# Kernel optimization log

Measured on AMD Instinct MI355X. Metric: run time of the kernel, lower is better.

Reference implementation:

```python
import jax, jax.numpy as jnp
import numpy as np

N = 4096      # number of nodes
C = 8         # channels (w1..w8 in source)
IN_DIM = 256  # input feature dim
D = 64        # per-channel dim (c_dim)
OUT = 128     # out_dim
ITERS = 4     # routing iterations
BETA = 1.0    # temperature
DENSITY = 0.01


def _l2norm(x):
    # tf.nn.l2_normalize along last axis with eps=1e-12
    return x * jax.lax.rsqrt(jnp.maximum(jnp.sum(x * x, axis=-1, keepdims=True), 1e-12))


def setup_inputs() -> dict:
    key = jax.random.key(0)
    k0, k1, k2, k3, k4, k5 = jax.random.split(key, 6)
    features = jax.random.normal(k0, (N, IN_DIM), dtype=jnp.float32)
    # sparse-ish 0/1 adjacency stored densely (as in the original model)
    adj = (jax.random.uniform(k1, (N, N)) < DENSITY).astype(jnp.float32)
    W = jax.random.normal(k2, (C, IN_DIM, D), dtype=jnp.float32)    # w1..w8 stacked
    b = jax.random.normal(k3, (C, 1, D), dtype=jnp.float32)         # b1..b8 stacked
    W_o = jax.random.normal(k4, (C * D, OUT), dtype=jnp.float32)
    bias = jax.random.normal(k5, (1, OUT), dtype=jnp.float32)
    return {"features": features, "adj": adj, "W": W, "b": b, "W_o": W_o, "bias": bias}


def reference(features, adj, W, b, W_o, bias):
    mask = adj > 0  # [N, N]
    # per-channel projection + l2 normalize: z[c] = l2norm(features @ w[c] + b[c])
    z = _l2norm(jnp.einsum('ni,cid->cnd', features, W) + b)  # [C, N, D]
    for _ in range(ITERS):
        # dense per-channel attention (XX^T), masked by adjacency
        A = jnp.einsum('cnd,cmd->cnm', z, z)                 # [C, N, N]
        A = jnp.where(mask[None], A, 0.0) / BETA
        # softmax across channels at each (i, j), then re-mask
        A = jax.nn.softmax(A, axis=0)
        A = jnp.where(mask[None], A, 0.0)
        # aggregate + residual + l2 normalize
        z = _l2norm(z + jnp.einsum('cnm,cmd->cnd', A, z))
    # concat channels along feature axis: [N, C*D]
    h = jnp.transpose(z, (1, 0, 2)).reshape(N, C * D)
    # (dropout skipped: stochastic op, identity in the deterministic reference)
    return h @ W_o + bias
```

## Files before the change

kernel.cpp:

```cpp
#include <hip/hip_runtime.h>
#include <hip/hip_bf16.h>

#define N_NODES 4096
#define C_CH    8
#define IN_DIM  256
#define D_DIM   64
#define CD      512
#define OUT_DIM 128
#define ITERS   4
#define STRIDE  128

typedef __hip_bfloat16 bf16;
typedef short short8 __attribute__((ext_vector_type(8)));
typedef float floatx4 __attribute__((ext_vector_type(4)));

__device__ __forceinline__ float bf2f(bf16 x) { return __bfloat162float(x); }

__device__ __forceinline__ unsigned f2b_rne(float x) {
    unsigned u = __float_as_uint(x);
    return (u + 0x7FFFu + ((u >> 16) & 1u)) >> 16;
}
__device__ __forceinline__ unsigned pack2bf(float a, float b) {
    return f2b_rne(a) | (f2b_rne(b) << 16);
}
__device__ __forceinline__ void unpack2(unsigned v, float& a, float& b) {
    a = __uint_as_float(v << 16);
    b = __uint_as_float(v & 0xFFFF0000u);
}
__device__ __forceinline__ short8 as_s8(uint4 u) {
    union { uint4 a; short8 b; } x; x.a = u; return x.b;
}

__device__ __forceinline__ bool wave_detect(const unsigned* __restrict__ feat_u) {
    int lane = threadIdx.x & 63;
    unsigned u = feat_u[lane];
    int e = (u >> 7) & 0xFF;
    int vote = (e >= 0x68 && e <= 0x86) ? 1 : 0;
    #pragma unroll
    for (int off = 32; off; off >>= 1) vote += __shfl_xor(vote, off);
    return vote >= 32;
}

__global__ __launch_bounds__(256) void mega_pre(
        const void* __restrict__ feat, const void* __restrict__ adj,
        const void* __restrict__ W, const void* __restrict__ b,
        const void* __restrict__ Wo,
        unsigned* __restrict__ zbf, int* __restrict__ deg,
        int* __restrict__ col_buf, unsigned short* __restrict__ Wo_t) {
    bool isbf = wave_detect((const unsigned*)feat);
    int bx = blockIdx.x;
    int t = threadIdx.x;

    if (bx < 512) {
        int nb = bx * 8;
        __shared__ float fs[8 * IN_DIM];
        if (isbf) {
            const uint4* p = (const uint4*)((const unsigned short*)feat + (size_t)nb * IN_DIM);
            uint4 u = p[t];
            float v[8];
            unpack2(u.x, v[0], v[1]); unpack2(u.y, v[2], v[3]);
            unpack2(u.z, v[4], v[5]); unpack2(u.w, v[6], v[7]);
            *(float4*)&fs[t * 8]     = make_float4(v[0], v[1], v[2], v[3]);
            *(float4*)&fs[t * 8 + 4] = make_float4(v[4], v[5], v[6], v[7]);
        } else {
            const float4* p = (const float4*)((const float*)feat + (size_t)nb * IN_DIM);
            float4 u0 = p[t];
            float4 u1 = p[t + 256];
            *(float4*)&fs[t * 4]         = u0;
            *(float4*)&fs[(t + 256) * 4] = u1;
        }
        __syncthreads();

        int d = t & 63;
        size_t wbase0 = (size_t)(t >> 6) * IN_DIM * D_DIM + d;
        size_t wbase1 = (size_t)(4 + (t >> 6)) * IN_DIM * D_DIM + d;
        float a0[8] = {}, a1[8] = {};
        for (int k = 0; k < IN_DIM; k++) {
            float w0, w1;
            if (isbf) {
                w0 = bf2f(((const bf16*)W)[wbase0 + k * D_DIM]);
                w1 = bf2f(((const bf16*)W)[wbase1 + k * D_DIM]);
            } else {
                w0 = ((const float*)W)[wbase0 + k * D_DIM];
                w1 = ((const float*)W)[wbase1 + k * D_DIM];
            }
            #pragma unroll
            for (int r = 0; r < 8; r++) {
                float f = fs[r * IN_DIM + k];
                a0[r] = fmaf(f, w0, a0[r]);
                a1[r] = fmaf(f, w1, a1[r]);
            }
        }
        float b0 = isbf ? bf2f(((const bf16*)b)[t])       : ((const float*)b)[t];
        float b1 = isbf ? bf2f(((const bf16*)b)[256 + t]) : ((const float*)b)[256 + t];

        #pragma unroll
        for (int r = 0; r < 8; r++) {
            float v0 = a0[r] + b0;
            float v1 = a1[r] + b1;
            float ss0 = v0 * v0, ss1 = v1 * v1;
            #pragma unroll
            for (int off = 32; off; off >>= 1) {
                ss0 += __shfl_xor(ss0, off);
                ss1 += __shfl_xor(ss1, off);
            }
            float o0 = v0 * __builtin_amdgcn_rsqf(fmaxf(ss0, 1e-12f));
            float o1 = v1 * __builtin_amdgcn_rsqf(fmaxf(ss1, 1e-12f));
            size_t row = (size_t)(nb + r);
            float p0 = __shfl_xor(o0, 1);
            float p1 = __shfl_xor(o1, 1);
            if (!(t & 1)) {
                zbf[row * 256 + (t >> 1)]       = pack2bf(o0, p0);
                zbf[row * 256 + 128 + (t >> 1)] = pack2bf(o1, p1);
            }
        }
    } else if (bx < 1536) {
        int w = t >> 6, lane = t & 63;
        int i = (bx - 512) * 4 + w;
        int base_out = i * STRIDE;
        int running = 0;
        int nch = isbf ? 8 : 16;
        for (int ch = 0; ch < nch; ch++) {
            unsigned bits = 0;
            int j0, nelem;
            if (isbf) {
                const uint4* p = (const uint4*)((const unsigned short*)adj + (size_t)i * N_NODES);
                uint4 u = p[ch * 64 + lane];
                j0 = (ch * 64 + lane) * 8; nelem = 8;
                unsigned short h[8] = {
                    (unsigned short)(u.x & 0xFFFF), (unsigned short)(u.x >> 16),
                    (unsigned short)(u.y & 0xFFFF), (unsigned short)(u.y >> 16),
                    (unsigned short)(u.z & 0xFFFF), (unsigned short)(u.z >> 16),
                    (unsigned short)(u.w & 0xFFFF), (unsigned short)(u.w >> 16)};
                #pragma unroll
                for (int k = 0; k < 8; k++)
                    if ((h[k] & 0x8000) == 0 && h[k] != 0) bits |= (1u << k);
            } else {
                const float4* p = (const float4*)((const float*)adj + (size_t)i * N_NODES);
                float4 f = p[ch * 64 + lane];
                j0 = (ch * 64 + lane) * 4; nelem = 4;
                if (f.x > 0.f) bits |= 1u;
                if (f.y > 0.f) bits |= 2u;
                if (f.z > 0.f) bits |= 4u;
                if (f.w > 0.f) bits |= 8u;
            }
            int cnt = __popc(bits);
            int sc = cnt;
            #pragma unroll
            for (int off = 1; off < 64; off <<= 1) {
                int v = __shfl_up(sc, off);
                if (lane >= off) sc += v;
            }
            int tot = __shfl(sc, 63);
            int pos = base_out + running + (sc - cnt);
            for (int k = 0; k < nelem; k++) {
                if ((bits >> k) & 1u) {
                    if (pos < base_out + STRIDE) col_buf[pos] = j0 + k;
                    pos++;
                }
            }
            running += tot;
        }
        if ((t & 63) == 0) deg[i] = (running < STRIDE) ? running : STRIDE;
    } else {
        int idx = (bx - 1536) * 256 + t;
        int n = idx & 127;
        int k = idx >> 7;
        unsigned short v;
        if (isbf) v = ((const unsigned short*)Wo)[idx];
        else      v = (unsigned short)f2b_rne(((const float*)Wo)[idx]);
        Wo_t[n * CD + k] = v;
    }
}

__device__ __forceinline__ void edge_step(const float zi[8], float acc[8], uint4 u) {
    float vj[8];
    unpack2(u.x, vj[0], vj[1]);
    unpack2(u.y, vj[2], vj[3]);
    unpack2(u.z, vj[4], vj[5]);
    unpack2(u.w, vj[6], vj[7]);
    float p = 0.f;
    #pragma unroll
    for (int k = 0; k < 8; k++) p = fmaf(zi[k], vj[k], p);
    p += __shfl_xor(p, 1); p += __shfl_xor(p, 2); p += __shfl_xor(p, 4);
    float ex = __expf(p);
    float s = ex;
    s += __shfl_xor(s, 8); s += __shfl_xor(s, 16); s += __shfl_xor(s, 32);
    float wgt = ex * __builtin_amdgcn_rcpf(s);
    #pragma unroll
    for (int k = 0; k < 8; k++) acc[k] = fmaf(wgt, vj[k], acc[k]);
}

__global__ __launch_bounds__(256) void route_kernel(
        const unsigned* __restrict__ zbf_in, unsigned* __restrict__ zbf_out,
        const int* __restrict__ deg, const int* __restrict__ col_buf) {
    int w = threadIdx.x >> 6, lane = threadIdx.x & 63;
    int pair = w >> 1;
    int half = w & 1;
    int i = blockIdx.x * 2 + pair;
    int g = lane >> 3, s = lane & 7;
    __shared__ int   s_cols[2][STRIDE];
    __shared__ float s_acc[2][CD];

    s_cols[pair][half * 64 + lane] = col_buf[i * STRIDE + half * 64 + lane];
    __syncthreads();

    int frag = g * 32 + s * 4;
    uint4 uown = *(const uint4*)(zbf_in + (size_t)i * 256 + frag);
    float zi[8], acc[8];
    unpack2(uown.x, zi[0], zi[1]); unpack2(uown.y, zi[2], zi[3]);
    unpack2(uown.z, zi[4], zi[5]); unpack2(uown.w, zi[6], zi[7]);
    #pragma unroll
    for (int k = 0; k < 8; k++) acc[k] = half ? 0.f : zi[k];

    int dg = deg[i];
    int e_mid = (dg + 1) >> 1;
    int e   = half ? e_mid : 0;
    int end = half ? dg    : e_mid;
    for (; e + 3 < end; e += 4) {
        int j0 = s_cols[pair][e]     & (N_NODES - 1);
        int j1 = s_cols[pair][e + 1] & (N_NODES - 1);
        int j2 = s_cols[pair][e + 2] & (N_NODES - 1);
        int j3 = s_cols[pair][e + 3] & (N_NODES - 1);
        uint4 u0 = *(const uint4*)(zbf_in + (size_t)j0 * 256 + frag);
        uint4 u1 = *(const uint4*)(zbf_in + (size_t)j1 * 256 + frag);
        uint4 u2 = *(const uint4*)(zbf_in + (size_t)j2 * 256 + frag);
        uint4 u3 = *(const uint4*)(zbf_in + (size_t)j3 * 256 + frag);
        edge_step(zi, acc, u0);
        edge_step(zi, acc, u1);
        edge_step(zi, acc, u2);
        edge_step(zi, acc, u3);
    }
    for (; e < end; e++) {
        int j0 = s_cols[pair][e] & (N_NODES - 1);
        uint4 u0 = *(const uint4*)(zbf_in + (size_t)j0 * 256 + frag);
        edge_step(zi, acc, u0);
    }

    int flat = g * D_DIM + s * 8;
    if (half) {
        *(float4*)&s_acc[pair][flat]     = make_float4(acc[0], acc[1], acc[2], acc[3]);
        *(float4*)&s_acc[pair][flat + 4] = make_float4(acc[4], acc[5], acc[6], acc[7]);
    }
    __syncthreads();
    if (!half) {
        float4 p0 = *(const float4*)&s_acc[pair][flat];
        float4 p1 = *(const float4*)&s_acc[pair][flat + 4];
        acc[0] += p0.x; acc[1] += p0.y; acc[2] += p0.z; acc[3] += p0.w;
        acc[4] += p1.x; acc[5] += p1.y; acc[6] += p1.z; acc[7] += p1.w;

        float ss = 0.f;
        #pragma unroll
        for (int k = 0; k < 8; k++) ss = fmaf(acc[k], acc[k], ss);
        ss += __shfl_xor(ss, 1); ss += __shfl_xor(ss, 2); ss += __shfl_xor(ss, 4);
        float sc = __builtin_amdgcn_rsqf(fmaxf(ss, 1e-12f));
        float o[8];
        #pragma unroll
        for (int k = 0; k < 8; k++) o[k] = acc[k] * sc;

        uint4 ob;
        ob.x = pack2bf(o[0], o[1]); ob.y = pack2bf(o[2], o[3]);
        ob.z = pack2bf(o[4], o[5]); ob.w = pack2bf(o[6], o[7]);
        *(uint4*)(zbf_out + (size_t)i * 256 + frag) = ob;
    }
}

__global__ __launch_bounds__(256) void out_gemm_mfma(
        const unsigned* __restrict__ zbf, const unsigned* __restrict__ wot_u,
        const void* __restrict__ bias, void* __restrict__ out,
        const void* __restrict__ feat) {
    bool isbf = wave_detect((const unsigned*)feat);
    int w = threadIdx.x >> 6, lane = threadIdx.x & 63;
    int r0 = blockIdx.x * 32 + (w & 1) * 16;
    int n0 = (w >> 1) * 64;
    int m = lane & 15, quad = lane >> 4;

    floatx4 acc0 = {0.f, 0.f, 0.f, 0.f}, acc1 = acc0, acc2 = acc0, acc3 = acc0;
    const unsigned* ap  = zbf   + (size_t)(r0 + m) * 256 + quad * 4;
    const unsigned* bp0 = wot_u + (size_t)(n0 + m) * 256 + quad * 4;
    const unsigned* bp1 = bp0 + 16 * 256;
    const unsigned* bp2 = bp0 + 32 * 256;
    const unsigned* bp3 = bp0 + 48 * 256;

    #pragma unroll
    for (int k0 = 0; k0 < 256; k0 += 16) {
        short8 a  = as_s8(*(const uint4*)(ap  + k0));
        short8 b0 = as_s8(*(const uint4*)(bp0 + k0));
        short8 b1 = as_s8(*(const uint4*)(bp1 + k0));
        short8 b2 = as_s8(*(const uint4*)(bp2 + k0));
        short8 b3 = as_s8(*(const uint4*)(bp3 + k0));
        acc0 = __builtin_amdgcn_mfma_f32_16x16x32_bf16(a, b0, acc0, 0, 0, 0);
        acc1 = __builtin_amdgcn_mfma_f32_16x16x32_bf16(a, b1, acc1, 0, 0, 0);
        acc2 = __builtin_amdgcn_mfma_f32_16x16x32_bf16(a, b2, acc2, 0, 0, 0);
        acc3 = __builtin_amdgcn_mfma_f32_16x16x32_bf16(a, b3, acc3, 0, 0, 0);
    }

    float accs[4][4] = {
        {acc0[0], acc0[1], acc0[2], acc0[3]},
        {acc1[0], acc1[1], acc1[2], acc1[3]},
        {acc2[0], acc2[1], acc2[2], acc2[3]},
        {acc3[0], acc3[1], acc3[2], acc3[3]}};
    #pragma unroll
    for (int c = 0; c < 4; c++) {
        int col = n0 + c * 16 + m;
        float bb = isbf ? bf2f(((const bf16*)bias)[col]) : ((const float*)bias)[col];
        #pragma unroll
        for (int r = 0; r < 4; r++) {
            int row = r0 + quad * 4 + r;
            float v = accs[c][r] + bb;
            size_t oi = (size_t)row * OUT_DIM + col;
            if (isbf) ((bf16*)out)[oi] = __float2bfloat16(v);
            else      ((float*)out)[oi] = v;
        }
    }
}

extern "C" void kernel_launch(void* const* d_in, const int* in_sizes, int n_in,
                              void* d_out, int out_size, void* d_ws, size_t ws_size,
                              hipStream_t stream) {
    const void* feat = d_in[0];
    const void* adj  = d_in[1];
    const void* W    = d_in[2];
    const void* b    = d_in[3];
    const void* Wo   = d_in[4];
    const void* bias = d_in[5];

    char* ws = (char*)d_ws;
    unsigned*       zbf_a   = (unsigned*)ws;
    unsigned*       zbf_b   = (unsigned*)(ws + (4u << 20));
    unsigned short* Wo_t    = (unsigned short*)(ws + (8u << 20));
    int*            deg     = (int*)(ws + (9u << 20));
    int*            col_buf = (int*)(ws + (9u << 20) + (64u << 10));

    mega_pre<<<1792, 256, 0, stream>>>(feat, adj, W, b, Wo,
                                       zbf_a, deg, col_buf, Wo_t);

    unsigned* bin = zbf_a;
    unsigned* bot = zbf_b;
    for (int it = 0; it < ITERS; it++) {
        route_kernel<<<N_NODES / 2, 256, 0, stream>>>(bin, bot, deg, col_buf);
        unsigned* tb = bin; bin = bot; bot = tb;
    }
    out_gemm_mfma<<<N_NODES / 32, 256, 0, stream>>>(zbf_a, (const unsigned*)Wo_t,
                                                    bias, d_out, feat);
}
```

Baseline: 234.1 us.

## Use MFMA for channel projection and split routing edges across four waves

The scalar FMA projection of features onto the eight channel weights is replaced by a bf16 MFMA GEMM. A new pre-stage transposes W into a K-contiguous bf16 layout and also handles the W_o transpose. The routing kernel now assigns one node per block and splits its edges across four waves instead of two, reducing the partials through shared memory. This targets the slow scalar projection and the latency-bound gather loop, at the cost of an extra launch and more bf16 rounding of the features.

```diff
diff --git a/kernel.cpp b/kernel.cpp
--- a/kernel.cpp
+++ b/kernel.cpp
@@ -41,82 +41,162 @@
     return vote >= 32;
 }
 
-__global__ __launch_bounds__(256) void mega_pre(
+__global__ __launch_bounds__(256) void stage_a(
+        const void* __restrict__ feat, const void* __restrict__ W,
+        const void* __restrict__ Wo,
+        unsigned short* __restrict__ Wt, unsigned short* __restrict__ Wo_t) {
+    bool isbf = wave_detect((const unsigned*)feat);
+    int bx = blockIdx.x, t = threadIdx.x;
+    if (bx < 8) {
+        __shared__ __align__(16) unsigned short lt[IN_DIM * D_DIM];
+        int c = bx;
+        if (isbf) {
+            const uint4* p = (const uint4*)((const unsigned short*)W + (size_t)c * IN_DIM * D_DIM);
+            #pragma unroll
+            for (int i = 0; i < 8; i++) {
+                int idx = t + i * 256;
+                *(uint4*)&lt[idx * 8] = p[idx];
+            }
+        } else {
+            const float4* p = (const float4*)((const float*)W + (size_t)c * IN_DIM * D_DIM);
+            #pragma unroll
+            for (int i = 0; i < 16; i++) {
+                int idx = t + i * 256;
+                float4 f = p[idx];
+                uint2 v = make_uint2(pack2bf(f.x, f.y), pack2bf(f.z, f.w));
+                *(uint2*)&lt[idx * 4] = v;
+            }
+        }
+        __syncthreads();
+        uint4* wt4 = (uint4*)Wt;
+        #pragma unroll
+        for (int i = 0; i < 8; i++) {
+            int j = t + i * 256;
+            int d = j >> 5, seg = j & 31;
+            int k0 = seg * 8;
+            unsigned short v[8];
+            #pragma unroll
+            for (int k = 0; k < 8; k++) v[k] = lt[(k0 + k) * D_DIM + d];
+            uint4 o;
+            o.x = v[0] | ((unsigned)v[1] << 16);
+            o.y = v[2] | ((unsigned)v[3] << 16);
+            o.z = v[4] | ((unsigned)v[5] << 16);
+            o.w = v[6] | ((unsigned)v[7] << 16);
+            wt4[(c * 64 + d) * 32 + seg] = o;
+        }
+    } else {
+        int base = (bx - 8) * 1024 + t * 4;
+        #pragma unroll
+        for (int q = 0; q < 4; q++) {
+            int idx = base + q;
+            int k = idx >> 7, n = idx & 127;
+            unsigned short v;
+            if (isbf) v = ((const unsigned short*)Wo)[idx];
+            else      v = (unsigned short)f2b_rne(((const float*)Wo)[idx]);
+            Wo_t[n * CD + k] = v;
+        }
+    }
+}
+
+__global__ __launch_bounds__(256) void stage_b(
         const void* __restrict__ feat, const void* __restrict__ adj,
-        const void* __restrict__ W, const void* __restrict__ b,
-        const void* __restrict__ Wo,
+        const void* __restrict__ b, const unsigned short* __restrict__ Wt,
         unsigned* __restrict__ zbf, int* __restrict__ deg,
-        int* __restrict__ col_buf, unsigned short* __restrict__ Wo_t) {
+        int* __restrict__ col_buf) {
     bool isbf = wave_detect((const unsigned*)feat);
-    int bx = blockIdx.x;
-    int t = threadIdx.x;
-
-    if (bx < 512) {
-        int nb = bx * 8;
-        __shared__ float fs[8 * IN_DIM];
+    int bx = blockIdx.x, t = threadIdx.x;
+    int w = t >> 6, lane = t & 63;
+    __shared__ __align__(16) unsigned short zt[16 * CD];
+
+    if (bx < 256) {
+        int r0 = bx * 16;
+        int n0 = w * 128;
+        int m = lane & 15, quad = lane >> 4;
+        int row = r0 + m;
+        floatx4 acc[8];
+        #pragma unroll
+        for (int j = 0; j < 8; j++) acc[j] = (floatx4){0.f, 0.f, 0.f, 0.f};
+        const uint4* wt4 = (const uint4*)Wt;
+
         if (isbf) {
-            const uint4* p = (const uint4*)((const unsigned short*)feat + (size_t)nb * IN_DIM);
-            uint4 u = p[t];
-            float v[8];
-            unpack2(u.x, v[0], v[1]); unpack2(u.y, v[2], v[3]);
-            unpack2(u.z, v[4], v[5]); unpack2(u.w, v[6], v[7]);
-            *(float4*)&fs[t * 8]     = make_float4(v[0], v[1], v[2], v[3]);
-            *(float4*)&fs[t * 8 + 4] = make_float4(v[4], v[5], v[6], v[7]);
+            const uint4* a4 = (const uint4*)feat + (size_t)row * 32 + quad;
+            #pragma unroll
+            for (int k0 = 0; k0 < 8; k0++) {
+                short8 a = as_s8(a4[k0 * 4]);
+                #pragma unroll
+                for (int j = 0; j < 8; j++) {
+                    int col = n0 + j * 16 + m;
+                    short8 bb = as_s8(wt4[col * 32 + k0 * 4 + quad]);
+                    acc[j] = __builtin_amdgcn_mfma_f32_16x16x32_bf16(a, bb, acc[j], 0, 0, 0);
+                }
+            }
         } else {
-            const float4* p = (const float4*)((const float*)feat + (size_t)nb * IN_DIM);
-            float4 u0 = p[t];
-            float4 u1 = p[t + 256];
-            *(float4*)&fs[t * 4]         = u0;
-            *(float4*)&fs[(t + 256) * 4] = u1;
+            const float4* a4 = (const float4*)feat + (size_t)row * 64 + quad * 2;
+            #pragma unroll
+            for (int k0 = 0; k0 < 8; k0++) {
+                float4 f0 = a4[k0 * 8], f1 = a4[k0 * 8 + 1];
+                uint4 au;
+                au.x = pack2bf(f0.x, f0.y); au.y = pack2bf(f0.z, f0.w);
+                au.z = pack2bf(f1.x, f1.y); au.w = pack2bf(f1.z, f1.w);
+                short8 a = as_s8(au);
+                #pragma unroll
+                for (int j = 0; j < 8; j++) {
+                    int col = n0 + j * 16 + m;
+                    short8 bb = as_s8(wt4[col * 32 + k0 * 4 + quad]);
+                    acc[j] = __builtin_amdgcn_mfma_f32_16x16x32_bf16(a, bb, acc[j], 0, 0, 0);
+                }
+            }
+        }
+
+        float pre[8][4];
+        #pragma unroll
+        for (int j = 0; j < 8; j++) {
+            int col = n0 + j * 16 + m;
+            float bb = isbf ? bf2f(((const bf16*)b)[col]) : ((const float*)b)[col];
+            #pragma unroll
+            for (int r = 0; r < 4; r++) pre[j][r] = acc[j][r] + bb;
+        }
+        #pragma unroll
+        for (int ch = 0; ch < 2; ch++) {
+            float ss[4];
+            #pragma unroll
+            for (int r = 0; r < 4; r++) {
+                float s = 0.f;
+                #pragma unroll
+                for (int jj = 0; jj < 4; jj++) {
+                    float v = pre[ch * 4 + jj][r];
+                    s = fmaf(v, v, s);
+                }
+                ss[r] = s;
+            }
+            #pragma unroll
+            for (int off = 1; off < 16; off <<= 1) {
+                #pragma unroll
+                for (int r = 0; r < 4; r++) ss[r] += __shfl_xor(ss[r], off);
+            }
+            #pragma unroll
+            for (int r = 0; r < 4; r++) {
+                float sc = __builtin_amdgcn_rsqf(fmaxf(ss[r], 1e-12f));
+                int lrow = quad * 4 + r;
+                #pragma unroll
+                for (int jj = 0; jj < 4; jj++) {
+                    int j = ch * 4 + jj;
+                    int col = n0 + j * 16 + m;
+                    zt[lrow * CD + col] = (unsigned short)f2b_rne(pre[j][r] * sc);
+                }
+            }
         }
         __syncthreads();
-
-        int d = t & 63;
-        size_t wbase0 = (size_t)(t >> 6) * IN_DIM * D_DIM + d;
-        size_t wbase1 = (size_t)(4 + (t >> 6)) * IN_DIM * D_DIM + d;
-        float a0[8] = {}, a1[8] = {};
-        for (int k = 0; k < IN_DIM; k++) {
-            float w0, w1;
-            if (isbf) {
-                w0 = bf2f(((const bf16*)W)[wbase0 + k * D_DIM]);
-                w1 = bf2f(((const bf16*)W)[wbase1 + k * D_DIM]);
-            } else {
-                w0 = ((const float*)W)[wbase0 + k * D_DIM];
-                w1 = ((const float*)W)[wbase1 + k * D_DIM];
-            }
-            #pragma unroll
-            for (int r = 0; r < 8; r++) {
-                float f = fs[r * IN_DIM + k];
-                a0[r] = fmaf(f, w0, a0[r]);
-                a1[r] = fmaf(f, w1, a1[r]);
-            }
-        }
-        float b0 = isbf ? bf2f(((const bf16*)b)[t])       : ((const float*)b)[t];
-        float b1 = isbf ? bf2f(((const bf16*)b)[256 + t]) : ((const float*)b)[256 + t];
-
-        #pragma unroll
-        for (int r = 0; r < 8; r++) {
-            float v0 = a0[r] + b0;
-            float v1 = a1[r] + b1;
-            float ss0 = v0 * v0, ss1 = v1 * v1;
-            #pragma unroll
-            for (int off = 32; off; off >>= 1) {
-                ss0 += __shfl_xor(ss0, off);
-                ss1 += __shfl_xor(ss1, off);
-            }
-            float o0 = v0 * __builtin_amdgcn_rsqf(fmaxf(ss0, 1e-12f));
-            float o1 = v1 * __builtin_amdgcn_rsqf(fmaxf(ss1, 1e-12f));
-            size_t row = (size_t)(nb + r);
-            float p0 = __shfl_xor(o0, 1);
-            float p1 = __shfl_xor(o1, 1);
-            if (!(t & 1)) {
-                zbf[row * 256 + (t >> 1)]       = pack2bf(o0, p0);
-                zbf[row * 256 + 128 + (t >> 1)] = pack2bf(o1, p1);
-            }
-        }
-    } else if (bx < 1536) {
-        int w = t >> 6, lane = t & 63;
-        int i = (bx - 512) * 4 + w;
+        const uint4* zt4 = (const uint4*)zt;
+        uint4* z4 = (uint4*)zbf;
+        #pragma unroll
+        for (int i = 0; i < 4; i++) {
+            int j = t + i * 256;
+            int lrow = j >> 6, seg = j & 63;
+            z4[(size_t)(r0 + lrow) * 64 + seg] = zt4[j];
+        }
+    } else {
+        int i = (bx - 256) * 4 + w;
         int base_out = i * STRIDE;
         int running = 0;
         int nch = isbf ? 8 : 16;
@@ -161,15 +241,7 @@
             }
             running += tot;
         }
-        if ((t & 63) == 0) deg[i] = (running < STRIDE) ? running : STRIDE;
-    } else {
-        int idx = (bx - 1536) * 256 + t;
-        int n = idx & 127;
-        int k = idx >> 7;
-        unsigned short v;
-        if (isbf) v = ((const unsigned short*)Wo)[idx];
-        else      v = (unsigned short)f2b_rne(((const float*)Wo)[idx]);
-        Wo_t[n * CD + k] = v;
+        if (lane == 0) deg[i] = (running < STRIDE) ? running : STRIDE;
     }
 }
 
@@ -194,15 +266,13 @@
 __global__ __launch_bounds__(256) void route_kernel(
         const unsigned* __restrict__ zbf_in, unsigned* __restrict__ zbf_out,
         const int* __restrict__ deg, const int* __restrict__ col_buf) {
-    int w = threadIdx.x >> 6, lane = threadIdx.x & 63;
-    int pair = w >> 1;
-    int half = w & 1;
-    int i = blockIdx.x * 2 + pair;
+    int t = threadIdx.x;
+    int w = t >> 6, lane = t & 63;
+    int i = blockIdx.x;
     int g = lane >> 3, s = lane & 7;
-    __shared__ int   s_cols[2][STRIDE];
-    __shared__ float s_acc[2][CD];
-
-    s_cols[pair][half * 64 + lane] = col_buf[i * STRIDE + half * 64 + lane];
+    __shared__ int   s_cols[STRIDE];
+    __shared__ float s_acc[3][CD];
+    if (t < STRIDE) s_cols[t] = col_buf[i * STRIDE + t];
     __syncthreads();
 
     int frag = g * 32 + s * 4;
@@ -211,17 +281,16 @@
     unpack2(uown.x, zi[0], zi[1]); unpack2(uown.y, zi[2], zi[3]);
     unpack2(uown.z, zi[4], zi[5]); unpack2(uown.w, zi[6], zi[7]);
     #pragma unroll
-    for (int k = 0; k < 8; k++) acc[k] = half ? 0.f : zi[k];
+    for (int k = 0; k < 8; k++) acc[k] = (w == 0) ? zi[k] : 0.f;
 
     int dg = deg[i];
-    int e_mid = (dg + 1) >> 1;
-    int e   = half ? e_mid : 0;
-    int end = half ? dg    : e_mid;
+    int e   = (dg * w) >> 2;
+    int end = (dg * (w + 1)) >> 2;
     for (; e + 3 < end; e += 4) {
-        int j0 = s_cols[pair][e]     & (N_NODES - 1);
-        int j1 = s_cols[pair][e + 1] & (N_NODES - 1);
-        int j2 = s_cols[pair][e + 2] & (N_NODES - 1);
-        int j3 = s_cols[pair][e + 3] & (N_NODES - 1);
+        int j0 = s_cols[e]     & (N_NODES - 1);
+        int j1 = s_cols[e + 1] & (N_NODES - 1);
+        int j2 = s_cols[e + 2] & (N_NODES - 1);
+        int j3 = s_cols[e + 3] & (N_NODES - 1);
         uint4 u0 = *(const uint4*)(zbf_in + (size_t)j0 * 256 + frag);
         uint4 u1 = *(const uint4*)(zbf_in + (size_t)j1 * 256 + frag);
         uint4 u2 = *(const uint4*)(zbf_in + (size_t)j2 * 256 + frag);
@@ -232,23 +301,25 @@
         edge_step(zi, acc, u3);
     }
     for (; e < end; e++) {
-        int j0 = s_cols[pair][e] & (N_NODES - 1);
+        int j0 = s_cols[e] & (N_NODES - 1);
         uint4 u0 = *(const uint4*)(zbf_in + (size_t)j0 * 256 + frag);
         edge_step(zi, acc, u0);
     }
 
     int flat = g * D_DIM + s * 8;
-    if (half) {
-        *(float4*)&s_acc[pair][flat]     = make_float4(acc[0], acc[1], acc[2], acc[3]);
-        *(float4*)&s_acc[pair][flat + 4] = make_float4(acc[4], acc[5], acc[6], acc[7]);
+    if (w) {
+        *(float4*)&s_acc[w - 1][flat]     = make_float4(acc[0], acc[1], acc[2], acc[3]);
+        *(float4*)&s_acc[w - 1][flat + 4] = make_float4(acc[4], acc[5], acc[6], acc[7]);
     }
     __syncthreads();
-    if (!half) {
-        float4 p0 = *(const float4*)&s_acc[pair][flat];
-        float4 p1 = *(const float4*)&s_acc[pair][flat + 4];
-        acc[0] += p0.x; acc[1] += p0.y; acc[2] += p0.z; acc[3] += p0.w;
-        acc[4] += p1.x; acc[5] += p1.y; acc[6] += p1.z; acc[7] += p1.w;
-
+    if (w == 0) {
+        #pragma unroll
+        for (int q = 0; q < 3; q++) {
+            float4 p0 = *(const float4*)&s_acc[q][flat];
+            float4 p1 = *(const float4*)&s_acc[q][flat + 4];
+            acc[0] += p0.x; acc[1] += p0.y; acc[2] += p0.z; acc[3] += p0.w;
+            acc[4] += p1.x; acc[5] += p1.y; acc[6] += p1.z; acc[7] += p1.w;
+        }
         float ss = 0.f;
         #pragma unroll
         for (int k = 0; k < 8; k++) ss = fmaf(acc[k], acc[k], ss);
@@ -257,7 +328,6 @@
         float o[8];
         #pragma unroll
         for (int k = 0; k < 8; k++) o[k] = acc[k] * sc;
-
         uint4 ob;
         ob.x = pack2bf(o[0], o[1]); ob.y = pack2bf(o[2], o[3]);
         ob.z = pack2bf(o[4], o[5]); ob.w = pack2bf(o[6], o[7]);
@@ -328,17 +398,18 @@
     char* ws = (char*)d_ws;
     unsigned*       zbf_a   = (unsigned*)ws;
     unsigned*       zbf_b   = (unsigned*)(ws + (4u << 20));
-    unsigned short* Wo_t    = (unsigned short*)(ws + (8u << 20));
-    int*            deg     = (int*)(ws + (9u << 20));
-    int*            col_buf = (int*)(ws + (9u << 20) + (64u << 10));
-
-    mega_pre<<<1792, 256, 0, stream>>>(feat, adj, W, b, Wo,
-                                       zbf_a, deg, col_buf, Wo_t);
+    unsigned short* Wt      = (unsigned short*)(ws + (8u << 20));
+    unsigned short* Wo_t    = (unsigned short*)(ws + (8u << 20) + (256u << 10));
+    int*            deg     = (int*)(ws + (8u << 20) + (512u << 10));
+    int*            col_buf = (int*)(ws + (9u << 20));
+
+    stage_a<<<72, 256, 0, stream>>>(feat, W, Wo, Wt, Wo_t);
+    stage_b<<<1280, 256, 0, stream>>>(feat, adj, b, Wt, zbf_a, deg, col_buf);
 
     unsigned* bin = zbf_a;
     unsigned* bot = zbf_b;
     for (int it = 0; it < ITERS; it++) {
-        route_kernel<<<N_NODES / 2, 256, 0, stream>>>(bin, bot, deg, col_buf);
+        route_kernel<<<N_NODES, 256, 0, stream>>>(bin, bot, deg, col_buf);
         unsigned* tb = bin; bin = bot; bot = tb;
     }
     out_gemm_mfma<<<N_NODES / 32, 256, 0, stream>>>(zbf_a, (const unsigned*)Wo_t,
```

Result: faster. 219.6 us (-6.2%).
